# Optimization experiments

Hardware: AMD Instinct MI355X
Metric: run time of the kernel (lower is better)

The kernel has to match this reference:

```python
import jax, jax.numpy as jnp
import numpy as np

TOP_K = 2  # top_routing

def setup_inputs() -> dict:
    key = jax.random.key(0)
    ks = jax.random.split(key, 8)
    B, D, O, E = 2048, 1024, 1024, 8
    H = D * 10  # hidden_dim hard-coded as input_dim*10
    s_d = 1.0 / np.sqrt(D)
    s_h = 1.0 / np.sqrt(H)
    return {
        "x1": jax.random.normal(ks[0], (B, D), jnp.float32),
        "x2": jax.random.normal(ks[1], (B, D), jnp.float32),
        "gate_w": jax.random.uniform(ks[2], (E, D), jnp.float32, -s_d, s_d),
        "gate_b": jax.random.uniform(ks[3], (E,), jnp.float32, -s_d, s_d),
        "fc1_w": jax.random.uniform(ks[4], (E, H, D), jnp.float32, -s_d, s_d),
        "fc1_b": jax.random.uniform(ks[5], (E, H), jnp.float32, -s_d, s_d),
        "fc2_w": jax.random.uniform(ks[6], (E, O, H), jnp.float32, -s_h, s_h),
        "fc2_b": jax.random.uniform(ks[7], (E, O), jnp.float32, -s_h, s_h),
    }


def reference(x1, x2, gate_w, gate_b, fc1_w, fc1_b, fc2_w, fc2_b):
    # Gate: softmax over experts, then top-k sparsify (values kept, rest zeroed)
    gate_logits = x1 @ gate_w.T + gate_b                    # [B, E]
    gate_probs = jax.nn.softmax(gate_logits, axis=1)
    top_vals, top_idx = jax.lax.top_k(gate_probs, TOP_K)    # [B, K]
    B = gate_probs.shape[0]
    rows = jnp.arange(B)[:, None]
    gate_probs = jnp.zeros_like(gate_probs).at[rows, top_idx].set(top_vals)

    # All experts run densely on x2 (faithful to the original Python loop)
    hidden = jnp.einsum('bd,ehd->beh', x2, fc1_w) + fc1_b   # [B, E, H]
    hidden = jax.nn.relu(hidden)
    expert_out = jnp.einsum('beh,eoh->beo', hidden, fc2_w) + fc2_b  # [B, E, O]

    # bmm(gate_probs[:,None,:], expert_out).squeeze(1)
    return jnp.einsum('be,beo->bo', gate_probs, expert_out)  # [B, O]
```

## Files before the change

### kernel.cpp

```cpp
#include <hip/hip_runtime.h>
#include <hip/hip_fp16.h>

#define BTOK 2048
#define DIM 1024
#define ODIM 1024
#define NEXP 8
#define HID 10240
#define CAP 2048
#define KSPL 4

typedef _Float16 half8 __attribute__((ext_vector_type(8)));
typedef __fp16 fp16x2 __attribute__((ext_vector_type(2)));
typedef float floatx4 __attribute__((ext_vector_type(4)));

#define WS_HIDDEN_OFF 0
#define WS_COUNTS_OFF 83886080UL
#define WS_TOKENS_OFF 83886144UL
#define WS_PROBS_OFF  83951680UL
#define WS_NEEDED     84017216UL

__global__ void gate_kernel(const float* __restrict__ x1,
                            const float* __restrict__ gate_w,
                            const float* __restrict__ gate_b,
                            int* counts, int* tokens, float* probs) {
    int b = blockIdx.x;
    int lane = threadIdx.x;
    const float* xr = x1 + (size_t)b * DIM;
    float acc[NEXP];
#pragma unroll
    for (int e = 0; e < NEXP; e++) acc[e] = 0.f;
    for (int i = 0; i < DIM / 64; i++) {
        int d = lane + i * 64;
        float xv = xr[d];
#pragma unroll
        for (int e = 0; e < NEXP; e++) acc[e] += xv * gate_w[e * DIM + d];
    }
#pragma unroll
    for (int e = 0; e < NEXP; e++)
        for (int off = 32; off > 0; off >>= 1) acc[e] += __shfl_xor(acc[e], off);
    if (lane == 0) {
        float l[NEXP], m = -1e30f;
#pragma unroll
        for (int e = 0; e < NEXP; e++) { l[e] = acc[e] + gate_b[e]; m = fmaxf(m, l[e]); }
        float p[NEXP], s = 0.f;
#pragma unroll
        for (int e = 0; e < NEXP; e++) { p[e] = expf(l[e] - m); s += p[e]; }
        float inv = 1.f / s;
        int e0 = 0; float v0 = p[0];
#pragma unroll
        for (int e = 1; e < NEXP; e++) if (p[e] > v0) { v0 = p[e]; e0 = e; }
        int e1 = -1; float v1 = -1.f;
#pragma unroll
        for (int e = 0; e < NEXP; e++) if (e != e0 && p[e] > v1) { v1 = p[e]; e1 = e; }
        int pos0 = atomicAdd(&counts[e0], 1);
        tokens[e0 * CAP + pos0] = b; probs[e0 * CAP + pos0] = v0 * inv;
        int pos1 = atomicAdd(&counts[e1], 1);
        tokens[e1 * CAP + pos1] = b; probs[e1 * CAP + pos1] = v1 * inv;
    }
}

__global__ void offsets_kernel(const int* counts, int* offs) {
    if (threadIdx.x == 0) {
        int r = 0;
        for (int e = 0; e < NEXP; e++) { offs[e] = r; r += counts[e]; }
    }
}

#define BM 128
#define BN 128
#define BK 32
#define LDSS 40

__device__ __forceinline__ void cvt_store16(_Float16* dst, float4 a, float4 b,
                                            float4 c, float4 d) {
    union { fp16x2 h2[8]; half8 h8[2]; } u;
    u.h2[0] = __builtin_amdgcn_cvt_pkrtz(a.x, a.y);
    u.h2[1] = __builtin_amdgcn_cvt_pkrtz(a.z, a.w);
    u.h2[2] = __builtin_amdgcn_cvt_pkrtz(b.x, b.y);
    u.h2[3] = __builtin_amdgcn_cvt_pkrtz(b.z, b.w);
    u.h2[4] = __builtin_amdgcn_cvt_pkrtz(c.x, c.y);
    u.h2[5] = __builtin_amdgcn_cvt_pkrtz(c.z, c.w);
    u.h2[6] = __builtin_amdgcn_cvt_pkrtz(d.x, d.y);
    u.h2[7] = __builtin_amdgcn_cvt_pkrtz(d.z, d.w);
    *(half8*)dst = u.h8[0];
    *(half8*)(dst + 8) = u.h8[1];
}

__global__ __launch_bounds__(256, 2) void gemm1_kernel(
    const float* __restrict__ x2, const float* __restrict__ fc1_w,
    const float* __restrict__ fc1_b, const int* __restrict__ counts,
    const int* __restrict__ offs, const int* __restrict__ tokens,
    _Float16* __restrict__ hidden) {
    int d = blockIdx.x;
    int logical = (d & 7) * (gridDim.x >> 3) + (d >> 3);
    int mt = logical & 15;
    int rest = logical >> 4;
    int nt = rest % (HID / BN);
    int e = rest / (HID / BN);

    int cnt = counts[e];
    int m0 = mt * BM;
    if (m0 >= cnt) return;
    int n0 = nt * BN;
    int off = offs[e];

    __shared__ _Float16 As[BM][LDSS];
    __shared__ _Float16 Bs[BN][LDSS];

    int t = threadIdx.x, lane = t & 63, wave = t >> 6;
    int waveM = wave & 1, waveN = wave >> 1;
    int srow = t >> 1, shalf = t & 1;

    int arowc = min(m0 + srow, cnt - 1);
    int tok = tokens[e * CAP + arowc];
    const float* aptr = x2 + (size_t)tok * DIM + shalf * 16;
    const float* bptr = fc1_w + ((size_t)e * HID + n0 + srow) * DIM + shalf * 16;

    floatx4 acc[4][4];
#pragma unroll
    for (int mi = 0; mi < 4; mi++)
#pragma unroll
        for (int ni = 0; ni < 4; ni++) acc[mi][ni] = (floatx4){0.f, 0.f, 0.f, 0.f};

    int fr = lane & 15, quad = lane >> 4;
    float4 a0, a1, a2, a3, b0, b1, b2, b3;
    {
        const float4* ap = (const float4*)aptr;
        a0 = ap[0]; a1 = ap[1]; a2 = ap[2]; a3 = ap[3];
        const float4* bp = (const float4*)bptr;
        b0 = bp[0]; b1 = bp[1]; b2 = bp[2]; b3 = bp[3];
    }
    const int KT = DIM / BK;
    for (int kt = 0; kt < KT; kt++) {
        __syncthreads();
        cvt_store16(&As[srow][shalf * 16], a0, a1, a2, a3);
        cvt_store16(&Bs[srow][shalf * 16], b0, b1, b2, b3);
        __syncthreads();
        if (kt + 1 < KT) {
            const float4* ap = (const float4*)(aptr + (kt + 1) * BK);
            a0 = ap[0]; a1 = ap[1]; a2 = ap[2]; a3 = ap[3];
            const float4* bp = (const float4*)(bptr + (kt + 1) * BK);
            b0 = bp[0]; b1 = bp[1]; b2 = bp[2]; b3 = bp[3];
        }
        half8 af[4], bf[4];
#pragma unroll
        for (int mi = 0; mi < 4; mi++)
            af[mi] = *(const half8*)&As[waveM * 64 + mi * 16 + fr][quad * 8];
#pragma unroll
        for (int ni = 0; ni < 4; ni++)
            bf[ni] = *(const half8*)&Bs[waveN * 64 + ni * 16 + fr][quad * 8];
#pragma unroll
        for (int mi = 0; mi < 4; mi++)
#pragma unroll
            for (int ni = 0; ni < 4; ni++)
                acc[mi][ni] = __builtin_amdgcn_mfma_f32_16x16x32_f16(
                    af[mi], bf[ni], acc[mi][ni], 0, 0, 0);
    }
#pragma unroll
    for (int ni = 0; ni < 4; ni++) {
        int col = n0 + waveN * 64 + ni * 16 + fr;
        float bias = fc1_b[e * HID + col];
#pragma unroll
        for (int mi = 0; mi < 4; mi++) {
#pragma unroll
            for (int r = 0; r < 4; r++) {
                int rl = m0 + waveM * 64 + mi * 16 + quad * 4 + r;
                if (rl < cnt) {
                    float v = fmaxf(acc[mi][ni][r] + bias, 0.f);
                    hidden[(size_t)(off + rl) * HID + col] = (_Float16)v;
                }
            }
        }
    }
}

__global__ __launch_bounds__(256, 2) void gemm2_kernel(
    const _Float16* __restrict__ hidden, const float* __restrict__ fc2_w,
    const float* __restrict__ fc2_b, const int* __restrict__ counts,
    const int* __restrict__ offs, const int* __restrict__ tokens,
    const float* __restrict__ probs, float* __restrict__ out) {
    int d = blockIdx.x;
    int logical = (d & 7) * (gridDim.x >> 3) + (d >> 3);
    int mt = logical & 15;
    int rest = logical >> 4;
    int nt = rest & 7;
    int rest2 = rest >> 3;
    int ks = rest2 & (KSPL - 1);
    int e = rest2 >> 2;

    int cnt = counts[e];
    int m0 = mt * BM;
    if (m0 >= cnt) return;
    int n0 = nt * BN;
    int off = offs[e];
    int k0 = ks * (HID / KSPL);

    __shared__ _Float16 As[BM][LDSS];
    __shared__ _Float16 Bs[BN][LDSS];

    int t = threadIdx.x, lane = t & 63, wave = t >> 6;
    int waveM = wave & 1, waveN = wave >> 1;
    int srow = t >> 1, shalf = t & 1;

    int arowc = min(m0 + srow, cnt - 1);
    const _Float16* aptr = hidden + (size_t)(off + arowc) * HID + k0 + shalf * 16;
    const float* bptr = fc2_w + ((size_t)e * ODIM + n0 + srow) * HID + k0 + shalf * 16;

    floatx4 acc[4][4];
#pragma unroll
    for (int mi = 0; mi < 4; mi++)
#pragma unroll
        for (int ni = 0; ni < 4; ni++) acc[mi][ni] = (floatx4){0.f, 0.f, 0.f, 0.f};

    int fr = lane & 15, quad = lane >> 4;
    half8 ha0, ha1;
    float4 b0, b1, b2, b3;
    {
        ha0 = *(const half8*)aptr;
        ha1 = *(const half8*)(aptr + 8);
        const float4* bp = (const float4*)bptr;
        b0 = bp[0]; b1 = bp[1]; b2 = bp[2]; b3 = bp[3];
    }
    const int KT = (HID / KSPL) / BK;
    for (int kt = 0; kt < KT; kt++) {
        __syncthreads();
        *(half8*)&As[srow][shalf * 16] = ha0;
        *(half8*)&As[srow][shalf * 16 + 8] = ha1;
        cvt_store16(&Bs[srow][shalf * 16], b0, b1, b2, b3);
        __syncthreads();
        if (kt + 1 < KT) {
            ha0 = *(const half8*)(aptr + (kt + 1) * BK);
            ha1 = *(const half8*)(aptr + (kt + 1) * BK + 8);
            const float4* bp = (const float4*)(bptr + (kt + 1) * BK);
            b0 = bp[0]; b1 = bp[1]; b2 = bp[2]; b3 = bp[3];
        }
        half8 af[4], bf[4];
#pragma unroll
        for (int mi = 0; mi < 4; mi++)
            af[mi] = *(const half8*)&As[waveM * 64 + mi * 16 + fr][quad * 8];
#pragma unroll
        for (int ni = 0; ni < 4; ni++)
            bf[ni] = *(const half8*)&Bs[waveN * 64 + ni * 16 + fr][quad * 8];
#pragma unroll
        for (int mi = 0; mi < 4; mi++)
#pragma unroll
            for (int ni = 0; ni < 4; ni++)
                acc[mi][ni] = __builtin_amdgcn_mfma_f32_16x16x32_f16(
                    af[mi], bf[ni], acc[mi][ni], 0, 0, 0);
    }
#pragma unroll
    for (int ni = 0; ni < 4; ni++) {
        int col = n0 + waveN * 64 + ni * 16 + fr;
        float bias = (ks == 0) ? fc2_b[e * ODIM + col] : 0.f;
#pragma unroll
        for (int mi = 0; mi < 4; mi++) {
#pragma unroll
            for (int r = 0; r < 4; r++) {
                int rl = m0 + waveM * 64 + mi * 16 + quad * 4 + r;
                if (rl < cnt) {
                    float p = probs[e * CAP + rl];
                    int tok = tokens[e * CAP + rl];
                    atomicAdd(&out[(size_t)tok * ODIM + col],
                              p * (acc[mi][ni][r] + bias));
                }
            }
        }
    }
}

extern "C" void kernel_launch(void* const* d_in, const int* in_sizes, int n_in,
                              void* d_out, int out_size, void* d_ws, size_t ws_size,
                              hipStream_t stream) {
    if (ws_size < WS_NEEDED) return;
    const float* x1 = (const float*)d_in[0];
    const float* x2 = (const float*)d_in[1];
    const float* gate_w = (const float*)d_in[2];
    const float* gate_b = (const float*)d_in[3];
    const float* fc1_w = (const float*)d_in[4];
    const float* fc1_b = (const float*)d_in[5];
    const float* fc2_w = (const float*)d_in[6];
    const float* fc2_b = (const float*)d_in[7];
    float* out = (float*)d_out;
    char* ws = (char*)d_ws;
    _Float16* hidden = (_Float16*)(ws + WS_HIDDEN_OFF);
    int* counts = (int*)(ws + WS_COUNTS_OFF);
    int* offs = counts + NEXP;
    int* tokens = (int*)(ws + WS_TOKENS_OFF);
    float* probs = (float*)(ws + WS_PROBS_OFF);

    (void)hipMemsetAsync(counts, 0, 2 * NEXP * sizeof(int), stream);
    (void)hipMemsetAsync(d_out, 0, (size_t)out_size * sizeof(float), stream);
    gate_kernel<<<BTOK, 64, 0, stream>>>(x1, gate_w, gate_b, counts, tokens, probs);
    offsets_kernel<<<1, 64, 0, stream>>>(counts, offs);
    gemm1_kernel<<<(CAP / BM) * (HID / BN) * NEXP, 256, 0, stream>>>(
        x2, fc1_w, fc1_b, counts, offs, tokens, hidden);
    gemm2_kernel<<<(CAP / BM) * (ODIM / BN) * NEXP * KSPL, 256, 0, stream>>>(
        hidden, fc2_w, fc2_b, counts, offs, tokens, probs, out);
}
```

Before: 1.341 ms.

## Load GEMM tiles directly global-to-LDS with swizzled fp32 staging

Both expert GEMMs now move A and B tiles straight from global memory into LDS using global_load_lds, skipping the register staging path. Operands stay fp32 in LDS (A of gemm2 stays fp16) and are converted to fp16 when fragments are read, with an XOR swizzle to avoid bank conflicts. Launch bounds are raised to three blocks per CU. In exchange, LDS traffic and footprint double for the fp32 tiles, the conversion work repeats across waves, and the loop has only one LDS buffer, so overlap depends on the async load landing before the next barrier.

```diff
diff --git a/kernel.cpp b/kernel.cpp
--- a/kernel.cpp
+++ b/kernel.cpp
@@ -1,5 +1,6 @@
 #include <hip/hip_runtime.h>
 #include <hip/hip_fp16.h>
+#include <stdint.h>
 
 #define BTOK 2048
 #define DIM 1024
@@ -18,6 +19,12 @@
 #define WS_TOKENS_OFF 83886144UL
 #define WS_PROBS_OFF  83951680UL
 #define WS_NEEDED     84017216UL
+
+typedef __attribute__((address_space(1))) const unsigned int guint;
+typedef __attribute__((address_space(3))) unsigned int luint;
+__device__ __forceinline__ void gload16(const void* g, void* l) {
+    __builtin_amdgcn_global_load_lds((guint*)g, (luint*)l, 16, 0, 0);
+}
 
 __global__ void gate_kernel(const float* __restrict__ x1,
                             const float* __restrict__ gate_w,
@@ -69,24 +76,17 @@
 #define BM 128
 #define BN 128
 #define BK 32
-#define LDSS 40
-
-__device__ __forceinline__ void cvt_store16(_Float16* dst, float4 a, float4 b,
-                                            float4 c, float4 d) {
-    union { fp16x2 h2[8]; half8 h8[2]; } u;
+
+__device__ __forceinline__ half8 cvt8(float4 a, float4 b) {
+    union { fp16x2 h2[4]; half8 h8; } u;
     u.h2[0] = __builtin_amdgcn_cvt_pkrtz(a.x, a.y);
     u.h2[1] = __builtin_amdgcn_cvt_pkrtz(a.z, a.w);
     u.h2[2] = __builtin_amdgcn_cvt_pkrtz(b.x, b.y);
     u.h2[3] = __builtin_amdgcn_cvt_pkrtz(b.z, b.w);
-    u.h2[4] = __builtin_amdgcn_cvt_pkrtz(c.x, c.y);
-    u.h2[5] = __builtin_amdgcn_cvt_pkrtz(c.z, c.w);
-    u.h2[6] = __builtin_amdgcn_cvt_pkrtz(d.x, d.y);
-    u.h2[7] = __builtin_amdgcn_cvt_pkrtz(d.z, d.w);
-    *(half8*)dst = u.h8[0];
-    *(half8*)(dst + 8) = u.h8[1];
-}
-
-__global__ __launch_bounds__(256, 2) void gemm1_kernel(
+    return u.h8;
+}
+
+__global__ __launch_bounds__(256, 3) void gemm1_kernel(
     const float* __restrict__ x2, const float* __restrict__ fc1_w,
     const float* __restrict__ fc1_b, const int* __restrict__ counts,
     const int* __restrict__ offs, const int* __restrict__ tokens,
@@ -104,17 +104,25 @@
     int n0 = nt * BN;
     int off = offs[e];
 
-    __shared__ _Float16 As[BM][LDSS];
-    __shared__ _Float16 Bs[BN][LDSS];
+    __shared__ __align__(16) float As[BM * BK];
+    __shared__ __align__(16) float Bs[BN * BK];
 
     int t = threadIdx.x, lane = t & 63, wave = t >> 6;
     int waveM = wave & 1, waveN = wave >> 1;
-    int srow = t >> 1, shalf = t & 1;
-
-    int arowc = min(m0 + srow, cnt - 1);
-    int tok = tokens[e * CAP + arowc];
-    const float* aptr = x2 + (size_t)tok * DIM + shalf * 16;
-    const float* bptr = fc1_w + ((size_t)e * HID + n0 + srow) * DIM + shalf * 16;
+
+    int srow = t >> 3;
+    int sg = (t & 7) ^ (srow & 7);
+    const char* abase[4];
+#pragma unroll
+    for (int i = 0; i < 4; i++) {
+        int row = i * 32 + srow;
+        int arow = min(m0 + row, cnt - 1);
+        int tok = tokens[e * CAP + arow];
+        abase[i] = (const char*)(x2 + (size_t)tok * DIM + sg * 4);
+    }
+    const char* bbase = (const char*)(fc1_w + ((size_t)e * HID + n0 + srow) * DIM + sg * 4);
+    char* asd = (char*)As + wave * 1024;
+    char* bsd = (char*)Bs + wave * 1024;
 
     floatx4 acc[4][4];
 #pragma unroll
@@ -122,33 +130,39 @@
 #pragma unroll
         for (int ni = 0; ni < 4; ni++) acc[mi][ni] = (floatx4){0.f, 0.f, 0.f, 0.f};
 
-    int fr = lane & 15, quad = lane >> 4;
-    float4 a0, a1, a2, a3, b0, b1, b2, b3;
-    {
-        const float4* ap = (const float4*)aptr;
-        a0 = ap[0]; a1 = ap[1]; a2 = ap[2]; a3 = ap[3];
-        const float4* bp = (const float4*)bptr;
-        b0 = bp[0]; b1 = bp[1]; b2 = bp[2]; b3 = bp[3];
+    int fr = lane & 15, q = lane >> 4;
+#pragma unroll
+    for (int i = 0; i < 4; i++) {
+        gload16(abase[i], asd + i * 4096);
+        gload16(bbase + i * (32 * DIM * 4), bsd + i * 4096);
     }
     const int KT = DIM / BK;
     for (int kt = 0; kt < KT; kt++) {
         __syncthreads();
-        cvt_store16(&As[srow][shalf * 16], a0, a1, a2, a3);
-        cvt_store16(&Bs[srow][shalf * 16], b0, b1, b2, b3);
+        half8 af[4], bf[4];
+#pragma unroll
+        for (int mi = 0; mi < 4; mi++) {
+            int row = waveM * 64 + mi * 16 + fr;
+            float4 f0 = *(const float4*)((const char*)As + row * 128 + ((2 * q) ^ (row & 7)) * 16);
+            float4 f1 = *(const float4*)((const char*)As + row * 128 + ((2 * q + 1) ^ (row & 7)) * 16);
+            af[mi] = cvt8(f0, f1);
+        }
+#pragma unroll
+        for (int ni = 0; ni < 4; ni++) {
+            int row = waveN * 64 + ni * 16 + fr;
+            float4 f0 = *(const float4*)((const char*)Bs + row * 128 + ((2 * q) ^ (row & 7)) * 16);
+            float4 f1 = *(const float4*)((const char*)Bs + row * 128 + ((2 * q + 1) ^ (row & 7)) * 16);
+            bf[ni] = cvt8(f0, f1);
+        }
         __syncthreads();
         if (kt + 1 < KT) {
-            const float4* ap = (const float4*)(aptr + (kt + 1) * BK);
-            a0 = ap[0]; a1 = ap[1]; a2 = ap[2]; a3 = ap[3];
-            const float4* bp = (const float4*)(bptr + (kt + 1) * BK);
-            b0 = bp[0]; b1 = bp[1]; b2 = bp[2]; b3 = bp[3];
-        }
-        half8 af[4], bf[4];
-#pragma unroll
-        for (int mi = 0; mi < 4; mi++)
-            af[mi] = *(const half8*)&As[waveM * 64 + mi * 16 + fr][quad * 8];
-#pragma unroll
-        for (int ni = 0; ni < 4; ni++)
-            bf[ni] = *(const half8*)&Bs[waveN * 64 + ni * 16 + fr][quad * 8];
+            int koff = (kt + 1) * 128;
+#pragma unroll
+            for (int i = 0; i < 4; i++) {
+                gload16(abase[i] + koff, asd + i * 4096);
+                gload16(bbase + i * (32 * DIM * 4) + koff, bsd + i * 4096);
+            }
+        }
 #pragma unroll
         for (int mi = 0; mi < 4; mi++)
 #pragma unroll
@@ -164,7 +178,7 @@
         for (int mi = 0; mi < 4; mi++) {
 #pragma unroll
             for (int r = 0; r < 4; r++) {
-                int rl = m0 + waveM * 64 + mi * 16 + quad * 4 + r;
+                int rl = m0 + waveM * 64 + mi * 16 + q * 4 + r;
                 if (rl < cnt) {
                     float v = fmaxf(acc[mi][ni][r] + bias, 0.f);
                     hidden[(size_t)(off + rl) * HID + col] = (_Float16)v;
@@ -174,7 +188,7 @@
     }
 }
 
-__global__ __launch_bounds__(256, 2) void gemm2_kernel(
+__global__ __launch_bounds__(256, 3) void gemm2_kernel(
     const _Float16* __restrict__ hidden, const float* __restrict__ fc2_w,
     const float* __restrict__ fc2_b, const int* __restrict__ counts,
     const int* __restrict__ offs, const int* __restrict__ tokens,
@@ -195,16 +209,26 @@
     int off = offs[e];
     int k0 = ks * (HID / KSPL);
 
-    __shared__ _Float16 As[BM][LDSS];
-    __shared__ _Float16 Bs[BN][LDSS];
+    __shared__ __align__(16) _Float16 Ash[BM * BK];
+    __shared__ __align__(16) float Bs[BN * BK];
 
     int t = threadIdx.x, lane = t & 63, wave = t >> 6;
     int waveM = wave & 1, waveN = wave >> 1;
-    int srow = t >> 1, shalf = t & 1;
-
-    int arowc = min(m0 + srow, cnt - 1);
-    const _Float16* aptr = hidden + (size_t)(off + arowc) * HID + k0 + shalf * 16;
-    const float* bptr = fc2_w + ((size_t)e * ODIM + n0 + srow) * HID + k0 + shalf * 16;
+
+    int sarow = t >> 2;
+    int sag = (t & 3) ^ ((sarow >> 1) & 3);
+    const char* abase[2];
+#pragma unroll
+    for (int i = 0; i < 2; i++) {
+        int row = i * 64 + sarow;
+        int arow = min(m0 + row, cnt - 1);
+        abase[i] = (const char*)(hidden + (size_t)(off + arow) * HID + k0 + sag * 8);
+    }
+    int sbrow = t >> 3;
+    int sbg = (t & 7) ^ (sbrow & 7);
+    const char* bbase = (const char*)(fc2_w + ((size_t)e * ODIM + n0 + sbrow) * HID + k0 + sbg * 4);
+    char* asd = (char*)Ash + wave * 1024;
+    char* bsd = (char*)Bs + wave * 1024;
 
     floatx4 acc[4][4];
 #pragma unroll
@@ -212,35 +236,37 @@
 #pragma unroll
         for (int ni = 0; ni < 4; ni++) acc[mi][ni] = (floatx4){0.f, 0.f, 0.f, 0.f};
 
-    int fr = lane & 15, quad = lane >> 4;
-    half8 ha0, ha1;
-    float4 b0, b1, b2, b3;
-    {
-        ha0 = *(const half8*)aptr;
-        ha1 = *(const half8*)(aptr + 8);
-        const float4* bp = (const float4*)bptr;
-        b0 = bp[0]; b1 = bp[1]; b2 = bp[2]; b3 = bp[3];
-    }
+    int fr = lane & 15, q = lane >> 4;
+#pragma unroll
+    for (int i = 0; i < 2; i++) gload16(abase[i], asd + i * 4096);
+#pragma unroll
+    for (int i = 0; i < 4; i++) gload16(bbase + i * (32 * HID * 4), bsd + i * 4096);
+
     const int KT = (HID / KSPL) / BK;
     for (int kt = 0; kt < KT; kt++) {
         __syncthreads();
-        *(half8*)&As[srow][shalf * 16] = ha0;
-        *(half8*)&As[srow][shalf * 16 + 8] = ha1;
-        cvt_store16(&Bs[srow][shalf * 16], b0, b1, b2, b3);
+        half8 af[4], bf[4];
+#pragma unroll
+        for (int mi = 0; mi < 4; mi++) {
+            int row = waveM * 64 + mi * 16 + fr;
+            af[mi] = *(const half8*)((const char*)Ash + row * 64 + (q ^ ((row >> 1) & 3)) * 16);
+        }
+#pragma unroll
+        for (int ni = 0; ni < 4; ni++) {
+            int row = waveN * 64 + ni * 16 + fr;
+            float4 f0 = *(const float4*)((const char*)Bs + row * 128 + ((2 * q) ^ (row & 7)) * 16);
+            float4 f1 = *(const float4*)((const char*)Bs + row * 128 + ((2 * q + 1) ^ (row & 7)) * 16);
+            bf[ni] = cvt8(f0, f1);
+        }
         __syncthreads();
         if (kt + 1 < KT) {
-            ha0 = *(const half8*)(aptr + (kt + 1) * BK);
-            ha1 = *(const half8*)(aptr + (kt + 1) * BK + 8);
-            const float4* bp = (const float4*)(bptr + (kt + 1) * BK);
-            b0 = bp[0]; b1 = bp[1]; b2 = bp[2]; b3 = bp[3];
-        }
-        half8 af[4], bf[4];
-#pragma unroll
-        for (int mi = 0; mi < 4; mi++)
-            af[mi] = *(const half8*)&As[waveM * 64 + mi * 16 + fr][quad * 8];
-#pragma unroll
-        for (int ni = 0; ni < 4; ni++)
-            bf[ni] = *(const half8*)&Bs[waveN * 64 + ni * 16 + fr][quad * 8];
+            int koffA = (kt + 1) * 64;
+            int koffB = (kt + 1) * 128;
+#pragma unroll
+            for (int i = 0; i < 2; i++) gload16(abase[i] + koffA, asd + i * 4096);
+#pragma unroll
+            for (int i = 0; i < 4; i++) gload16(bbase + i * (32 * HID * 4) + koffB, bsd + i * 4096);
+        }
 #pragma unroll
         for (int mi = 0; mi < 4; mi++)
 #pragma unroll
@@ -256,7 +282,7 @@
         for (int mi = 0; mi < 4; mi++) {
 #pragma unroll
             for (int r = 0; r < 4; r++) {
-                int rl = m0 + waveM * 64 + mi * 16 + quad * 4 + r;
+                int rl = m0 + waveM * 64 + mi * 16 + q * 4 + r;
                 if (rl < cnt) {
                     float p = probs[e * CAP + rl];
                     int tok = tokens[e * CAP + rl];
```

Result: faster. 1.268 ms (-5.5%).
